# Kernel optimization log

Measured on AMD Instinct MI355X. Metric: run time of the kernel, lower is better.

Reference implementation:

```python
import jax, jax.numpy as jnp
import numpy as np

V, D, F, H, NB, S, B = 16384, 512, 2048, 8, 4, 512, 2
T_STEPS = 3      # config.T: number of PC inference iterations
GAMMA = 0.1      # state-update step size


def _layernorm(x, s, b):
    m = x.mean(-1, keepdims=True)
    v = ((x - m) ** 2).mean(-1, keepdims=True)
    return (x - m) * jax.lax.rsqrt(v + 1e-5) * s + b


def setup_inputs() -> dict:
    key = jax.random.key(0)
    ks = jax.random.split(key, 12)
    r = lambda k, sh: jax.random.normal(k, sh, jnp.float32) * 0.02
    return {
        'word_emb': r(ks[0], (V, D)),
        'pos_emb': r(ks[1], (S, D)),
        'Wq': r(ks[2], (NB, D, D)),
        'Wk': r(ks[3], (NB, D, D)),
        'Wv': r(ks[4], (NB, D, D)),
        'bq': jnp.zeros((NB, D), jnp.float32),
        'bk': jnp.zeros((NB, D), jnp.float32),
        'bv': jnp.zeros((NB, D), jnp.float32),
        'Wo': r(ks[5], (NB, D, D)),
        'bo': jnp.zeros((NB, D), jnp.float32),
        'ln1_s': jnp.ones((NB, D), jnp.float32),
        'ln1_b': jnp.zeros((NB, D), jnp.float32),
        'ln2_s': jnp.ones((NB, D), jnp.float32),
        'ln2_b': jnp.zeros((NB, D), jnp.float32),
        'W1': r(ks[6], (NB, D, F)),
        'b1': jnp.zeros((NB, F), jnp.float32),
        'W2': r(ks[7], (NB, F, D)),
        'b2': jnp.zeros((NB, D), jnp.float32),
        'Wout': r(ks[8], (D, V)),
        'bout': jnp.zeros((V,), jnp.float32),
        'input_ids': jax.random.randint(ks[9], (B, S), 0, V),
        'target_ids': jax.random.randint(ks[10], (B, S), 0, V),
    }


def _forward(word_emb, pos_emb, Wq, Wk, Wv, bq, bk, bv, Wo, bo,
             ln1_s, ln1_b, ln2_s, ln2_b, W1, b1, W2, b2, Wout, bout,
             input_ids, target_ids):
    Bsz, Sl = input_ids.shape
    dh = D // H
    scale = 1.0 / float(np.sqrt(dh))
    ids = jnp.clip(input_ids, 0, V - 1)
    target = jax.nn.one_hot(jnp.clip(target_ids, 0, V - 1), V, dtype=word_emb.dtype)
    # bottom prediction: word + position embeddings
    mu_emb = word_emb[ids] + pos_emb[jnp.arange(Sl)][None]  # (B,S,D)
    causal = jnp.tril(jnp.ones((Sl, Sl), bool))
    neg = jnp.finfo(word_emb.dtype).min

    def attn(x, b):
        h = _layernorm(x, ln1_s[b], ln1_b[b])
        q = (h @ Wq[b] + bq[b]).reshape(Bsz, Sl, H, dh)
        k = (h @ Wk[b] + bk[b]).reshape(Bsz, Sl, H, dh)
        v = (h @ Wv[b] + bv[b]).reshape(Bsz, Sl, H, dh)
        sc = jnp.einsum('bqhd,bkhd->bhqk', q, k) * scale
        sc = jnp.where(causal, sc, neg)
        a = jax.nn.softmax(sc, axis=-1)
        return jnp.einsum('bhqk,bkhd->bqhd', a, v).reshape(Bsz, Sl, D)

    # generative functions g[l]: x_l -> mu_{l+1}; 4 PC layers per block
    # (pc_qkv->attn ctx, pc_output->Wo, pc_layer1->gelu(fc1), pc_layer2->fc2)
    gs = []
    for b in range(NB):
        gs.append(lambda x, b=b: attn(x, b))
        gs.append(lambda x, b=b: x @ Wo[b] + bo[b])
        gs.append(lambda x, b=b: jax.nn.gelu(_layernorm(x, ln2_s[b], ln2_b[b]) @ W1[b] + b1[b]))
        gs.append(lambda x, b=b: x @ W2[b] + b2[b])
    g_top = lambda x: x @ Wout + bout  # output pc layer -> logits mu

    # init_x: forward sweep sets each latent to its prediction
    xs = [mu_emb]
    for g in gs:
        xs.append(g(xs[-1]))
    L = len(gs)

    # T-step iterative PC inference: eps_l = x_l - mu_l, top clamped to target
    # x_l <- x_l + GAMMA * (J_{g_l}(x_l)^T eps_{l+1} - eps_l)
    for _ in range(T_STEPS):
        preds, vjps = [], []
        for l in range(L):
            mu, vj = jax.vjp(gs[l], xs[l])
            preds.append(mu)
            vjps.append(vj)
        logits, vj_top = jax.vjp(g_top, xs[L])
        eps = [xs[0] - mu_emb] + [xs[l + 1] - preds[l] for l in range(L)]
        eps_top = logits - target
        new_xs = []
        for l in range(L + 1):
            td = vjps[l](eps[l + 1])[0] if l < L else vj_top(eps_top)[0]
            new_xs.append(xs[l] + GAMMA * (td - eps[l]))
        xs = new_xs

    return g_top(xs[L])  # get_mu('linear_output')


def reference(word_emb, pos_emb, Wq, Wk, Wv, bq, bk, bv, Wo, bo,
              ln1_s, ln1_b, ln2_s, ln2_b, W1, b1, W2, b2, Wout, bout,
              input_ids, target_ids):
    return _forward(word_emb, pos_emb, Wq, Wk, Wv, bq, bk, bv, Wo, bo,
                    ln1_s, ln1_b, ln2_s, ln2_b, W1, b1, W2, b2, Wout, bout,
                    input_ids, target_ids)
```

## Files before the change

### kernel.cpp

```cpp
#include <hip/hip_runtime.h>
#include <hip/hip_bf16.h>
#include <math.h>

#define D_   512
#define F_   2048
#define V_   16384
#define H_   8
#define DH_  64
#define S_   512
#define B_   2
#define M_   1024
#define MD_  (M_ * D_)
#define MF_  (M_ * F_)
#define GAMMA_ 0.1f

typedef unsigned int u32;
typedef unsigned short u16;
typedef __attribute__((ext_vector_type(4))) float f32x4;
typedef __attribute__((ext_vector_type(8))) short s16x8;
typedef __attribute__((ext_vector_type(4))) u16 u16x4;
typedef __attribute__((ext_vector_type(8))) u16 u16x8;

__device__ __forceinline__ u16 f2b(float f) {
    __hip_bfloat16 h = __float2bfloat16(f);
    return *reinterpret_cast<u16*>(&h);
}
__device__ __forceinline__ float b2f(u16 v) {
    u32 u = ((u32)v) << 16;
    float f; __builtin_memcpy(&f, &u, 4); return f;
}
__device__ __forceinline__ u16x4 pack4(f32x4 v) {
    u16x4 o; o.x = f2b(v[0]); o.y = f2b(v[1]); o.z = f2b(v[2]); o.w = f2b(v[3]);
    return o;
}

__device__ __forceinline__ void gl_lds16(const void* g, void* l) {
    __builtin_amdgcn_global_load_lds((const __attribute__((address_space(1))) u32*)g,
                                     (__attribute__((address_space(3))) u32*)l, 16, 0, 0);
}

__device__ __forceinline__ float gelu_f(float v) {
    float u = 0.7978845608028654f * (v + 0.044715f * v * v * v);
    return 0.5f * v * (1.f + tanhf(u));
}

__device__ __forceinline__ f32x4 xpose4(f32x4 v, int b) {
#pragma unroll
    for (int s = 1; s < 4; s <<= 1) {
        f32x4 nv;
#pragma unroll
        for (int j = 0; j < 4; ++j) {
            float ex = __shfl_xor(v[j ^ s], s, 64);
            nv[j] = ((b ^ j) & s) ? ex : v[j];
        }
        v = nv;
    }
    return v;
}

__device__ __forceinline__ float wave_sum(float v) {
#pragma unroll
    for (int o = 32; o > 0; o >>= 1) v += __shfl_xor(v, o, 64);
    return v;
}

__device__ __forceinline__ void lds_barrier() {
    asm volatile("s_waitcnt lgkmcnt(0)" ::: "memory");
    __builtin_amdgcn_s_barrier();
    __builtin_amdgcn_sched_barrier(0);
}

#define E_F32   0
#define E_GELU  1
#define E_TD    2
#define E_QKV3  3
#define E_OUT   4
#define E_SYM   5

template<int BK>
__device__ __forceinline__ int swz(int c, int row) {
    if constexpr (BK == 32) return c ^ ((row >> 1) & 3);
    else                    return c ^ (row & 7);
}

template<int BM, int BN, int BK, int FM, int FN, int EPI>
__global__ __launch_bounds__(256)
void mfma_gemm(const u16* __restrict__ A, const u16* __restrict__ B,
               float* __restrict__ Cf, u16* __restrict__ Cb,
               u16* __restrict__ Cb2, u16* __restrict__ Cb3,
               const float* __restrict__ bias,
               int K, int lda, int ldb, int ldc,
               long sC, long sKz, float alpha,
               const float* __restrict__ base, const float* __restrict__ subv,
               const float* __restrict__ cvec, const u16* __restrict__ woutTb,
               const int* __restrict__ tcl,
               float* __restrict__ ebF, u16* __restrict__ ebB)
{
    constexpr int WC = BN / (FN * 16);
    static_assert((BM / (FM * 16)) * WC == 4, "4 waves");
    constexpr int LPR = BK / 8;
    constexpr int RPI = 2048 / BK;
    constexpr int NISS = BM / RPI + BN / RPI;
    if constexpr (EPI == E_SYM) {
        if (blockIdx.x > blockIdx.y) return;
    }
    __shared__ __align__(16) u16 Asl[3][BM * BK];
    __shared__ __align__(16) u16 Bsl[3][BN * BK];
    const int t = threadIdx.x, l = t & 63, wid = t >> 6;
    const int m0 = blockIdx.y * BM, n0 = blockIdx.x * BN;
    const long z = blockIdx.z;
    A += z * sKz;
    B += z * sKz;
    if (Cf) Cf += z * sC;

    f32x4 acc[FM][FN] = {};
    const int rm = (wid / WC) * (FM * 16), cn = (wid % WC) * (FN * 16);
    const int lr = l & 15, hi = l >> 4;
    const int srl = t / LPR, sc = t % LPR;

    auto stage = [&](int k0, int pb) {
#pragma unroll
        for (int i = 0; i < BM / RPI; ++i) {
            int row = i * RPI + srl;
            gl_lds16(A + (size_t)(m0 + row) * lda + k0 + swz<BK>(sc, row) * 8,
                     &Asl[pb][i * 2048 + t * 8]);
        }
#pragma unroll
        for (int i = 0; i < BN / RPI; ++i) {
            int row = i * RPI + srl;
            gl_lds16(B + (size_t)(n0 + row) * ldb + k0 + swz<BK>(sc, row) * 8,
                     &Bsl[pb][i * 2048 + t * 8]);
        }
    };
    auto compute = [&](int pb) {
#pragma unroll
        for (int kk = 0; kk < BK / 32; ++kk) {
            s16x8 av[FM], bv[FN];
#pragma unroll
            for (int fm = 0; fm < FM; ++fm)
                av[fm] = *(const s16x8*)&Asl[pb][(rm + fm * 16 + lr) * BK + swz<BK>(kk * 4 + hi, lr) * 8];
#pragma unroll
            for (int fn = 0; fn < FN; ++fn)
                bv[fn] = *(const s16x8*)&Bsl[pb][(cn + fn * 16 + lr) * BK + swz<BK>(kk * 4 + hi, lr) * 8];
#pragma unroll
            for (int fm = 0; fm < FM; ++fm)
#pragma unroll
                for (int fn = 0; fn < FN; ++fn)
                    acc[fm][fn] = __builtin_amdgcn_mfma_f32_16x16x32_bf16(av[fm], bv[fn], acc[fm][fn], 0, 0, 0);
        }
    };

    const int nst = K / BK;
    stage(0, 0);
    if (nst > 1) stage(BK, 1);
    int rd = 0, wr = 2;
    for (int s = 0; s < nst; ++s) {
        if (s < nst - 1)
            asm volatile("s_waitcnt vmcnt(%0)" :: "i"(NISS) : "memory");
        else
            asm volatile("s_waitcnt vmcnt(0)" ::: "memory");
        __builtin_amdgcn_s_barrier();
        __builtin_amdgcn_sched_barrier(0);
        compute(rd);
        if (s + 2 < nst) stage((s + 2) * BK, wr);
        rd = (rd + 1 == 3) ? 0 : rd + 1;
        wr = (wr + 1 == 3) ? 0 : wr + 1;
    }

    const int qb = lr & 3, qi = lr >> 2;
#pragma unroll
    for (int fm = 0; fm < FM; ++fm)
#pragma unroll
        for (int fn = 0; fn < FN; ++fn) {
            const int gm = m0 + rm + fm * 16 + hi * 4 + qb;
            const int gn0 = n0 + cn + fn * 16 + qi * 4;
            const size_t idx0 = (size_t)gm * ldc + gn0;
            if constexpr (EPI == E_QKV3) {
                const int gnf = n0 + cn + fn * 16;
                const int sel = gnf >> 9;
                if (sel < 2) {
                    f32x4 v = xpose4(acc[fm][fn], qb);
                    f32x4 bv4 = *(const f32x4*)&bias[gn0];
#pragma unroll
                    for (int j = 0; j < 4; ++j) v[j] += bv4[j];
                    int b = gm >> 9, s = gm & (S_ - 1);
                    int d9 = gn0 & 511, h = d9 >> 6, d = d9 & 63;
                    u16* dst = (sel == 0) ? Cb : Cb2;
                    *(u16x4*)&dst[(((size_t)(b * H_ + h) * S_ + s) << 6) + d] = pack4(v);
                } else {
                    const int gnl = gnf + lr;
                    const int gm0 = m0 + rm + fm * 16 + hi * 4;
                    int b = gm0 >> 9, s0 = gm0 & (S_ - 1);
                    int d9 = gnl & 511, h = d9 >> 6, d = d9 & 63;
                    float bb = bias[gnl];
                    f32x4 v = acc[fm][fn];
#pragma unroll
                    for (int j = 0; j < 4; ++j) v[j] += bb;
                    *(u16x4*)&Cb3[((((size_t)(b * H_ + h)) << 6) + d) * S_ + s0] = pack4(v);
                }
            } else if constexpr (EPI == E_SYM) {
                const int gnr = n0 + cn + fn * 16 + lr;
                const int mc0 = m0 + rm + fm * 16 + hi * 4;
                *(f32x4*)&Cf[(size_t)gnr * ldc + mc0] = acc[fm][fn];
                f32x4 v = xpose4(acc[fm][fn], qb);
                *(f32x4*)&Cf[idx0] = v;
            } else {
                f32x4 v = xpose4(acc[fm][fn], qb);
                if constexpr (EPI == E_F32) {
#pragma unroll
                    for (int j = 0; j < 4; ++j) v[j] *= alpha;
                    if (bias) {
                        f32x4 bv4 = *(const f32x4*)&bias[gn0];
#pragma unroll
                        for (int j = 0; j < 4; ++j) v[j] += bv4[j];
                    }
                    *(f32x4*)&Cf[idx0] = v;
                    if (Cb) *(u16x4*)&Cb[idx0] = pack4(v);
                } else if constexpr (EPI == E_OUT) {
                    f32x4 bv4 = *(const f32x4*)&bias[gn0];
#pragma unroll
                    for (int j = 0; j < 4; ++j) v[j] += bv4[j];
                    *(f32x4*)&Cf[idx0] = v;
                } else if constexpr (EPI == E_GELU) {
                    f32x4 bv4 = *(const f32x4*)&bias[gn0];
#pragma unroll
                    for (int j = 0; j < 4; ++j) v[j] = gelu_f(v[j] + bv4[j]);
                    *(u16x4*)&Cb[idx0] = pack4(v);
                } else if constexpr (EPI == E_TD) {
                    const int tc = tcl[gm];
                    f32x4 cv4 = *(const f32x4*)&cvec[gn0];
                    f32x4 ba4 = *(const f32x4*)&base[idx0];
                    u16x4 gv = *(const u16x4*)&woutTb[(size_t)tc * D_ + gn0];
                    f32x4 dlt, o2;
#pragma unroll
                    for (int j = 0; j < 4; ++j)
                        dlt[j] = GAMMA_ * (v[j] + cv4[j] - b2f(gv[j]));
                    if (subv) {
                        f32x4 sv4 = *(const f32x4*)&subv[idx0];
#pragma unroll
                        for (int j = 0; j < 4; ++j) dlt[j] -= GAMMA_ * sv4[j];
                    }
#pragma unroll
                    for (int j = 0; j < 4; ++j) o2[j] = ba4[j] + dlt[j];
                    if (Cf) *(f32x4*)&Cf[idx0] = o2;
                    *(u16x4*)&Cb[idx0] = pack4(o2);
                    if (ebF) *(f32x4*)&ebF[idx0] = dlt;
                    if (ebB) *(u16x4*)&ebB[idx0] = pack4(dlt);
                }
            }
        }
}

__global__ __launch_bounds__(256)
void tdec_kernel(const u16* __restrict__ xAb, const u16* __restrict__ Gb,
                 const u16* __restrict__ ebb, const u16* __restrict__ H2b,
                 const float* __restrict__ xAf, const float* __restrict__ ebf,
                 const float* __restrict__ x16f, const float* __restrict__ cvec,
                 const u16* __restrict__ woutTb, const int* __restrict__ tcl,
                 float* __restrict__ xBf, u16* __restrict__ xBb, float* __restrict__ ecf)
{
    constexpr int BM = 32, BN = 64, BK = 64;
    __shared__ __align__(16) u16 Asl[3][BM * BK];
    __shared__ __align__(16) u16 Bsl[3][BN * BK];
    const int t = threadIdx.x, l = t & 63, wid = t >> 6;
    const int m0 = blockIdx.y * BM, n0 = blockIdx.x * BN;
    f32x4 a1[2] = {}, a2[2] = {};
    const int rm = (wid >> 1) * 16, cn = (wid & 1) * 32;
    const int lr = l & 15, hi = l >> 4;
    const int srl = t >> 3, sc = t & 7;

    auto stage = [&](int s, int pb) {
        const u16* A = (s < 8) ? xAb : ebb;
        const u16* B = (s < 8) ? Gb : H2b;
        const int k0 = (s & 7) * BK;
        {
            int row = srl;
            gl_lds16(A + (size_t)(m0 + row) * D_ + k0 + swz<64>(sc, row) * 8,
                     &Asl[pb][t * 8]);
        }
#pragma unroll
        for (int i = 0; i < 2; ++i) {
            int row = i * 32 + srl;
            gl_lds16(B + (size_t)(n0 + row) * D_ + k0 + swz<64>(sc, row) * 8,
                     &Bsl[pb][i * 2048 + t * 8]);
        }
    };
    auto cmp = [&](int pb, f32x4 (&ac)[2]) {
#pragma unroll
        for (int kk = 0; kk < 2; ++kk) {
            s16x8 av = *(const s16x8*)&Asl[pb][(rm + lr) * BK + swz<64>(kk * 4 + hi, lr) * 8];
#pragma unroll
            for (int fn = 0; fn < 2; ++fn) {
                s16x8 bv = *(const s16x8*)&Bsl[pb][(cn + fn * 16 + lr) * BK + swz<64>(kk * 4 + hi, lr) * 8];
                ac[fn] = __builtin_amdgcn_mfma_f32_16x16x32_bf16(av, bv, ac[fn], 0, 0, 0);
            }
        }
    };

    stage(0, 0);
    stage(1, 1);
    int rd = 0, wr = 2;
    for (int s = 0; s < 16; ++s) {
        if (s < 15) asm volatile("s_waitcnt vmcnt(3)" ::: "memory");
        else        asm volatile("s_waitcnt vmcnt(0)" ::: "memory");
        __builtin_amdgcn_s_barrier();
        __builtin_amdgcn_sched_barrier(0);
        if (s < 8) cmp(rd, a1);
        else       cmp(rd, a2);
        if (s + 2 < 16) stage(s + 2, wr);
        rd = (rd + 1 == 3) ? 0 : rd + 1;
        wr = (wr + 1 == 3) ? 0 : wr + 1;
    }

    const int qb = lr & 3, qi = lr >> 2;
#pragma unroll
    for (int fn = 0; fn < 2; ++fn) {
        f32x4 v1 = xpose4(a1[fn], qb);
        f32x4 v2 = xpose4(a2[fn], qb);
        const int gm = m0 + rm + hi * 4 + qb;
        const int gn0 = n0 + cn + fn * 16 + qi * 4;
        const size_t idx0 = (size_t)gm * D_ + gn0;
        const int tc = tcl[gm];
        f32x4 cv4 = *(const f32x4*)&cvec[gn0];
        u16x4 gv = *(const u16x4*)&woutTb[(size_t)tc * D_ + gn0];
        f32x4 xa4 = *(const f32x4*)&xAf[idx0];
        f32x4 eb4 = *(const f32x4*)&ebf[idx0];
        f32x4 x164 = *(const f32x4*)&x16f[idx0];
        f32x4 xb4, ec4;
#pragma unroll
        for (int j = 0; j < 4; ++j) {
            float dlt = GAMMA_ * (v1[j] + cv4[j] - b2f(gv[j]) - eb4[j]);
            xb4[j] = xa4[j] + dlt;
            ec4[j] = xb4[j] - x164[j] - GAMMA_ * v2[j];
        }
        *(f32x4*)&xBf[idx0] = xb4;
        *(u16x4*)&xBb[idx0] = pack4(xb4);
        *(f32x4*)&ecf[idx0] = ec4;
    }
}

__global__ __launch_bounds__(128)
void flash_attn(const u16* __restrict__ q, const u16* __restrict__ k,
                const u16* __restrict__ vT, u16* __restrict__ ctx)
{
    __shared__ __align__(16) u16 Ks[3][64 * 64];
    __shared__ __align__(16) u16 Vs[3][64 * 64];
    __shared__ __align__(16) u16 Ps[2][16 * 64];
    const int t = threadIdx.x, l = t & 63, w = t >> 6;
    const int qt = blockIdx.x, z = blockIdx.y;
    const int bb = z >> 3, hh = z & 7;
    const int lr = l & 15, hi = l >> 4;
    const u16* qp = q + (((size_t)z * S_ + qt * 32 + w * 16) << 6);
    const u16* kp = k + ((size_t)z * S_ << 6);
    const u16* vp = vT + (((size_t)z) << 6) * S_;

    const s16x8 aq0 = *(const s16x8*)&qp[lr * 64 + hi * 8];
    const s16x8 aq1 = *(const s16x8*)&qp[lr * 64 + 32 + hi * 8];

    f32x4 o[4] = {};
    float m[4], ls[4];
#pragma unroll
    for (int r = 0; r < 4; ++r) { m[r] = -3.0e38f; ls[r] = 0.f; }
    const int qrow = qt * 32 + w * 16 + hi * 4;
    const int srow = t >> 3, scl = t & 7;
    const int cg = (scl ^ (srow & 7)) * 8;
    const int sw7 = (lr & 7);
    const int jmax = qt >> 1;

    auto stage = [&](int j, int pb) {
#pragma unroll
        for (int i = 0; i < 4; ++i)
            gl_lds16(kp + ((size_t)(j * 64 + i * 16 + srow) << 6) + cg,
                     &Ks[pb][i * 1024 + t * 8]);
#pragma unroll
        for (int i = 0; i < 4; ++i)
            gl_lds16(vp + (size_t)(i * 16 + srow) * S_ + j * 64 + cg,
                     &Vs[pb][i * 1024 + t * 8]);
    };

    stage(0, 0);
    if (jmax > 0) stage(1, 1);
    int rd = 0, wr = 2;
    for (int j = 0; j <= jmax; ++j) {
        if (j < jmax) asm volatile("s_waitcnt vmcnt(8)" ::: "memory");
        else          asm volatile("s_waitcnt vmcnt(0)" ::: "memory");
        __builtin_amdgcn_s_barrier();
        __builtin_amdgcn_sched_barrier(0);

        float pv[4][4];
        __builtin_amdgcn_s_setprio(1);
#pragma unroll
        for (int fn = 0; fn < 4; ++fn) {
            f32x4 acc = {};
            acc = __builtin_amdgcn_mfma_f32_16x16x32_bf16(aq0,
                    *(const s16x8*)&Ks[rd][((fn * 16 + lr) << 6) + ((hi ^ sw7) * 8)], acc, 0, 0, 0);
            acc = __builtin_amdgcn_mfma_f32_16x16x32_bf16(aq1,
                    *(const s16x8*)&Ks[rd][((fn * 16 + lr) << 6) + (((hi + 4) ^ sw7) * 8)], acc, 0, 0, 0);
#pragma unroll
            for (int r = 0; r < 4; ++r) pv[fn][r] = acc[r] * 0.125f;
        }
        __builtin_amdgcn_s_setprio(0);
        if (j == jmax) {
#pragma unroll
            for (int fn = 0; fn < 4; ++fn) {
                int col = j * 64 + fn * 16 + lr;
#pragma unroll
                for (int r = 0; r < 4; ++r)
                    if (col > qrow + r) pv[fn][r] = -3.0e38f;
            }
        }
        float sc[4], rs[4];
#pragma unroll
        for (int r = 0; r < 4; ++r) {
            float x = fmaxf(fmaxf(pv[0][r], pv[1][r]), fmaxf(pv[2][r], pv[3][r]));
#pragma unroll
            for (int off = 1; off < 16; off <<= 1) x = fmaxf(x, __shfl_xor(x, off, 64));
            float nm = fmaxf(m[r], x);
            sc[r] = expf(m[r] - nm);
            m[r] = nm;
            rs[r] = 0.f;
        }
#pragma unroll
        for (int fn = 0; fn < 4; ++fn)
#pragma unroll
            for (int r = 0; r < 4; ++r) {
                float p = expf(pv[fn][r] - m[r]);
                pv[fn][r] = p;
                rs[r] += p;
            }
#pragma unroll
        for (int r = 0; r < 4; ++r) {
#pragma unroll
            for (int off = 1; off < 16; off <<= 1) rs[r] += __shfl_xor(rs[r], off, 64);
            ls[r] = ls[r] * sc[r] + rs[r];
        }
#pragma unroll
        for (int fn = 0; fn < 4; ++fn)
#pragma unroll
            for (int r = 0; r < 4; ++r) o[fn][r] *= sc[r];
#pragma unroll
        for (int fn = 0; fn < 4; ++fn)
#pragma unroll
            for (int r = 0; r < 4; ++r) {
                int qr = hi * 4 + r;
                int ci = (2 * fn + (lr >> 3)) ^ (qr & 7);
                Ps[w][qr * 64 + ci * 8 + (lr & 7)] = f2b(pv[fn][r]);
            }
        __builtin_amdgcn_s_setprio(1);
#pragma unroll
        for (int ks = 0; ks < 2; ++ks) {
            const s16x8 pa = *(const s16x8*)&Ps[w][lr * 64 + (((4 * ks + hi) ^ sw7) * 8)];
#pragma unroll
            for (int fn = 0; fn < 4; ++fn)
                o[fn] = __builtin_amdgcn_mfma_f32_16x16x32_bf16(pa,
                        *(const s16x8*)&Vs[rd][((fn * 16 + lr) << 6) + (((hi + 4 * ks) ^ sw7) * 8)], o[fn], 0, 0, 0);
        }
        __builtin_amdgcn_s_setprio(0);
        if (j + 2 <= jmax) stage(j + 2, wr);
        rd = (rd + 1 == 3) ? 0 : rd + 1;
        wr = (wr + 1 == 3) ? 0 : wr + 1;
    }
    float inv[4];
#pragma unroll
    for (int r = 0; r < 4; ++r) inv[r] = 1.f / ls[r];
    u16* cp = ctx + ((size_t)(bb * S_ + qt * 32 + w * 16) * D_) + hh * 64;
    const int qb = lr & 3, qi = lr >> 2;
#pragma unroll
    for (int fn = 0; fn < 4; ++fn) {
        f32x4 v = o[fn];
#pragma unroll
        for (int r = 0; r < 4; ++r) v[r] *= inv[r];
        v = xpose4(v, qb);
        *(u16x4*)&cp[(size_t)(hi * 4 + qb) * D_ + fn * 16 + qi * 4] = pack4(v);
    }
}

__global__ __launch_bounds__(256)
void mega_prep(const float* __restrict__ Wq, const float* __restrict__ Wk,
               const float* __restrict__ Wv, const float* __restrict__ Wo,
               const float* __restrict__ W1, const float* __restrict__ W2,
               const float* __restrict__ Wout,
               const float* __restrict__ bq, const float* __restrict__ bk,
               const float* __restrict__ bv, const int* __restrict__ target_ids,
               const float* __restrict__ we, const float* __restrict__ pe,
               const int* __restrict__ input_ids,
               const float* __restrict__ ln1s0, const float* __restrict__ ln1b0,
               u16* __restrict__ wqkvT, u16* __restrict__ woT, u16* __restrict__ w1T,
               u16* __restrict__ w2T, u16* __restrict__ woutT,
               u16* __restrict__ woutD, float* __restrict__ qkvb, int* __restrict__ tcl,
               u16* __restrict__ h_b)
{
    __shared__ float tile[2][64][65];
    __shared__ float sh2[4];
    const int g = blockIdx.x, t = threadIdx.x;

    if (g >= 1281) {
        const int rr = (g - 1281) * 2 + (t >> 7);
        const int lc = t & 127;
        const int ss = rr & (S_ - 1);
        int id = input_ids[rr];
        id = id < 0 ? 0 : (id > V_ - 1 ? V_ - 1 : id);
        const float4 a = ((const float4*)we)[(size_t)id * 128 + lc];
        const float4 b = ((const float4*)pe)[(size_t)ss * 128 + lc];
        float4 x;
        x.x = a.x + b.x; x.y = a.y + b.y; x.z = a.z + b.z; x.w = a.w + b.w;
        const int w = t >> 6, wb = (t >> 7) << 1;
        float s = wave_sum(x.x + x.y + x.z + x.w);
        if ((t & 63) == 0) sh2[w] = s;
        __syncthreads();
        float mu = (sh2[wb] + sh2[wb + 1]) * (1.f / D_);
        float d0 = x.x - mu, d1 = x.y - mu, d2 = x.z - mu, d3 = x.w - mu;
        float qv = wave_sum(d0 * d0 + d1 * d1 + d2 * d2 + d3 * d3);
        __syncthreads();
        if ((t & 63) == 0) sh2[w] = qv;
        __syncthreads();
        float var = (sh2[wb] + sh2[wb + 1]) * (1.f / D_);
        float r = rsqrtf(var + 1e-5f);
        const int c0 = lc * 4;
        float4 scv = *(const float4*)&ln1s0[c0];
        float4 bbv = *(const float4*)&ln1b0[c0];
        f32x4 o;
        o[0] = d0 * r * scv.x + bbv.x; o[1] = d1 * r * scv.y + bbv.y;
        o[2] = d2 * r * scv.z + bbv.z; o[3] = d3 * r * scv.w + bbv.w;
        *(u16x4*)&h_b[(size_t)rr * D_ + c0] = pack4(o);
        return;
    }
    if (g == 1280) {
        for (int i = t; i < M_; i += 256) {
            int v = target_ids[i];
            tcl[i] = v < 0 ? 0 : (v > V_ - 1 ? V_ - 1 : v);
        }
        for (int i = t; i < 4 * 1536; i += 256) {
            int b = i / 1536, j = i - b * 1536;
            qkvb[i] = (j < 512) ? bq[b * 512 + j]
                    : (j < 1024) ? bk[b * 512 + j - 512] : bv[b * 512 + j - 1024];
        }
        return;
    }

    const float* in = nullptr;
    u16 *outT = nullptr, *outC = nullptr;
    int R = 512, C = 512, c0 = 0, rbase = 0;

    if (g < 192) {
        int sel = g / 64, rem = g % 64, zz = rem >> 4, st = (rem >> 1) & 7, hf = rem & 1;
        in = (sel == 0 ? Wq : sel == 1 ? Wk : Wv) + (size_t)zz * 262144;
        outT = wqkvT + (size_t)zz * 786432 + sel * 262144;
        c0 = st * 64; rbase = hf * 256;
    } else if (g < 256) {
        int rem = g - 192, zz = rem >> 4, st = (rem >> 1) & 7, hf = rem & 1;
        in = Wo + (size_t)zz * 262144; outT = woT + (size_t)zz * 262144;
        c0 = st * 64; rbase = hf * 256;
    } else if (g < 512) {
        int rem = g - 256, zz = rem >> 6, sub = rem & 63, st = sub >> 1, hf = sub & 1;
        in = W1 + (size_t)zz * 1048576; outT = w1T + (size_t)zz * 1048576;
        C = 2048; c0 = st * 64; rbase = hf * 256;
    } else if (g < 768) {
        int rem = g - 512, zz = rem >> 6, sub = rem & 63, st = sub & 7, ch = sub >> 3;
        in = W2 + (size_t)zz * 1048576; outT = w2T + (size_t)zz * 1048576;
        R = 2048; c0 = st * 64; rbase = ch * 256;
    } else {
        int rem = g - 768, st = rem >> 1, hf = rem & 1;
        in = Wout; outT = woutT; outC = woutD;
        C = 16384; c0 = st * 64; rbase = hf * 256;
    }

    const int lrow = t >> 4, lcol = (t & 15) * 4;
    float4 va[3][4];
    auto loadit = [&](int it, int slot) {
#pragma unroll
        for (int p = 0; p < 4; ++p)
            va[slot][p] = *(const float4*)&in[(size_t)(rbase + it * 64 + p * 16 + lrow) * C + c0 + lcol];
    };

    loadit(0, 0);
    loadit(1, 1);
#pragma unroll
    for (int it = 0; it < 4; ++it) {
        const int slot = it % 3;
        const int tb = it & 1;
        const int r0 = rbase + it * 64;
#pragma unroll
        for (int p = 0; p < 4; ++p) {
            float4 v = va[slot][p];
            int row = p * 16 + lrow;
            tile[tb][row][lcol] = v.x; tile[tb][row][lcol + 1] = v.y;
            tile[tb][row][lcol + 2] = v.z; tile[tb][row][lcol + 3] = v.w;
            if (outC) {
                f32x4 fv; fv[0] = v.x; fv[1] = v.y; fv[2] = v.z; fv[3] = v.w;
                *(u16x4*)&outC[(size_t)(r0 + row) * C + c0 + lcol] = pack4(fv);
            }
        }
        if (it < 2) loadit(it + 2, (it + 2) % 3);
        lds_barrier();
#pragma unroll
        for (int p = 0; p < 2; ++p) {
            int orow = p * 32 + (t >> 3), oc = (t & 7) * 8;
            u16x8 o;
#pragma unroll
            for (int j = 0; j < 8; ++j) o[j] = f2b(tile[tb][oc + j][orow]);
            *(u16x8*)&outT[(size_t)(c0 + orow) * R + r0 + oc] = o;
        }
    }
}

__global__ __launch_bounds__(256)
void gredcvec(const float* __restrict__ P, u16* __restrict__ G,
              const u16* __restrict__ woutD, const float* __restrict__ bout,
              float* __restrict__ cvec, const u16* __restrict__ w2T3,
              u16* __restrict__ H2)
{
    __shared__ __align__(16) u16 As2[3][32 * 64];
    __shared__ __align__(16) u16 Bs2[3][64 * 64];
    const int blk = blockIdx.x, t = threadIdx.x;
    if (blk < 1024) {
        int i = blk * 256 + t;
        float s = 0.f;
#pragma unroll
        for (int zz = 0; zz < 8; ++zz) s += P[(size_t)zz * D_ * D_ + i];
        G[i] = f2b(s);
    } else if (blk < 1152) {
        const int w = t >> 6, l = t & 63;
        const int d = (blk - 1024) * 4 + w;
        float s = 0.f;
        for (int it = 0; it < 32; ++it) {
            int base = it * 512 + l * 8;
            u16x8 wv = *(const u16x8*)&woutD[(size_t)d * V_ + base];
            float4 b0 = *(const float4*)&bout[base];
            float4 b1 = *(const float4*)&bout[base + 4];
            s += b2f(wv[0]) * b0.x + b2f(wv[1]) * b0.y + b2f(wv[2]) * b0.z + b2f(wv[3]) * b0.w
               + b2f(wv[4]) * b1.x + b2f(wv[5]) * b1.y + b2f(wv[6]) * b1.z + b2f(wv[7]) * b1.w;
        }
        s = wave_sum(s);
        if (l == 0) cvec[d] = s;
    } else {
        const int idx = blk - 1152;
        const int n0 = (idx & 7) * 64, m0 = (idx >> 3) * 32;
        const int l = t & 63, wid = t >> 6;
        const int lr = l & 15, hi = l >> 4;
        const int rm = (wid >> 1) * 16, cn = (wid & 1) * 32;
        const int srl = t >> 3, sc = t & 7;
        f32x4 acc2[2] = {};
        auto stg = [&](int s, int pb) {
            const int k0 = s * 64;
            gl_lds16(w2T3 + (size_t)(m0 + srl) * 2048 + k0 + swz<64>(sc, srl) * 8,
                     &As2[pb][t * 8]);
            gl_lds16(w2T3 + (size_t)(n0 + srl) * 2048 + k0 + swz<64>(sc, srl) * 8,
                     &Bs2[pb][t * 8]);
            gl_lds16(w2T3 + (size_t)(n0 + 32 + srl) * 2048 + k0 + swz<64>(sc, srl) * 8,
                     &Bs2[pb][2048 + t * 8]);
        };
        auto cmp = [&](int pb) {
#pragma unroll
            for (int kk = 0; kk < 2; ++kk) {
                s16x8 av = *(const s16x8*)&As2[pb][(rm + lr) * 64 + swz<64>(kk * 4 + hi, lr) * 8];
#pragma unroll
                for (int fn = 0; fn < 2; ++fn) {
                    s16x8 bv = *(const s16x8*)&Bs2[pb][(cn + fn * 16 + lr) * 64 + swz<64>(kk * 4 + hi, lr) * 8];
                    acc2[fn] = __builtin_amdgcn_mfma_f32_16x16x32_bf16(av, bv, acc2[fn], 0, 0, 0);
                }
            }
        };
        stg(0, 0);
        stg(1, 1);
        int rd = 0, wr = 2;
        for (int s = 0; s < 32; ++s) {
            if (s < 31) asm volatile("s_waitcnt vmcnt(3)" ::: "memory");
            else        asm volatile("s_waitcnt vmcnt(0)" ::: "memory");
            __builtin_amdgcn_s_barrier();
            __builtin_amdgcn_sched_barrier(0);
            cmp(rd);
            if (s + 2 < 32) stg(s + 2, wr);
            rd = (rd + 1 == 3) ? 0 : rd + 1;
            wr = (wr + 1 == 3) ? 0 : wr + 1;
        }
        const int qb = lr & 3, qi = lr >> 2;
#pragma unroll
        for (int fn = 0; fn < 2; ++fn) {
            f32x4 v = xpose4(acc2[fn], qb);
            const int gm = m0 + rm + hi * 4 + qb;
            const int gn0 = n0 + cn + fn * 16 + qi * 4;
            *(u16x4*)&H2[(size_t)gm * D_ + gn0] = pack4(v);
        }
    }
}

__global__ __launch_bounds__(256)
void ln_fwd_kernel(const float* __restrict__ x, const float* __restrict__ s,
                   const float* __restrict__ bb, u16* __restrict__ h)
{
    const int l = threadIdx.x & 63, w = threadIdx.x >> 6;
    const int row = blockIdx.x * 4 + w;
    const float* xr = x + (size_t)row * D_;
    const int c0 = l * 8;
    float4 a = *(const float4*)&xr[c0];
    float4 b = *(const float4*)&xr[c0 + 4];
    float sum = a.x + a.y + a.z + a.w + b.x + b.y + b.z + b.w;
    float mu = wave_sum(sum) * (1.f / D_);
    float d0 = a.x - mu, d1 = a.y - mu, d2 = a.z - mu, d3 = a.w - mu;
    float d4 = b.x - mu, d5 = b.y - mu, d6 = b.z - mu, d7 = b.w - mu;
    float vs = d0*d0 + d1*d1 + d2*d2 + d3*d3 + d4*d4 + d5*d5 + d6*d6 + d7*d7;
    float var = wave_sum(vs) * (1.f / D_);
    float r = rsqrtf(var + 1e-5f);
    float4 s0 = *(const float4*)&s[c0], s1 = *(const float4*)&s[c0 + 4];
    float4 b0 = *(const float4*)&bb[c0], b1 = *(const float4*)&bb[c0 + 4];
    u16* hr = h + (size_t)row * D_;
    f32x4 o0, o1;
    o0[0] = d0 * r * s0.x + b0.x; o0[1] = d1 * r * s0.y + b0.y;
    o0[2] = d2 * r * s0.z + b0.z; o0[3] = d3 * r * s0.w + b0.w;
    o1[0] = d4 * r * s1.x + b1.x; o1[1] = d5 * r * s1.y + b1.y;
    o1[2] = d6 * r * s1.z + b1.z; o1[3] = d7 * r * s1.w + b1.w;
    *(u16x4*)&hr[c0] = pack4(o0);
    *(u16x4*)&hr[c0 + 4] = pack4(o1);
}

extern "C" void kernel_launch(void* const* d_in, const int* in_sizes, int n_in,
                              void* d_out, int out_size, void* d_ws, size_t ws_size,
                              hipStream_t stream)
{
    (void)in_sizes; (void)n_in; (void)out_size;
    const float* Wq  = (const float*)d_in[2];
    const float* Wk  = (const float*)d_in[3];
    const float* Wv  = (const float*)d_in[4];
    const float* bq  = (const float*)d_in[5];
    const float* bk  = (const float*)d_in[6];
    const float* bv  = (const float*)d_in[7];
    const float* Wo  = (const float*)d_in[8];
    const float* bo  = (const float*)d_in[9];
    const float* ln1_s = (const float*)d_in[10];
    const float* ln1_b = (const float*)d_in[11];
    const float* ln2_s = (const float*)d_in[12];
    const float* ln2_b = (const float*)d_in[13];
    const float* W1  = (const float*)d_in[14];
    const float* b1  = (const float*)d_in[15];
    const float* W2  = (const float*)d_in[16];
    const float* b2  = (const float*)d_in[17];
    const float* Wout = (const float*)d_in[18];
    const float* bout = (const float*)d_in[19];
    const int* input_ids  = (const int*)d_in[20];
    const int* target_ids = (const int*)d_in[21];
    float* out = (float*)d_out;

    char* wsb = (char*)d_ws;
    size_t off = 0;
    auto alloc = [&](size_t bytes) -> void* {
        off = (off + 255) & ~(size_t)255;
        void* p = wsb + off; off += bytes; return p;
    };
    u16* wqkvT = (u16*)alloc((size_t)4 * 1536 * D_ * 2);
    u16* woT   = (u16*)alloc((size_t)4 * D_ * D_ * 2);
    u16* w1T   = (u16*)alloc((size_t)4 * D_ * F_ * 2);
    u16* w2T   = (u16*)alloc((size_t)4 * D_ * F_ * 2);
    u16* woutT = (u16*)alloc((size_t)V_ * D_ * 2);
    u16* G_b   = (u16*)alloc((size_t)D_ * D_ * 2);
    u16* H2_b  = (u16*)alloc((size_t)D_ * D_ * 2);
    float* qkvb = (float*)alloc((size_t)4 * 1536 * 4);
    float* bufB = (float*)alloc((size_t)MD_ * 4);
    u16* h_b    = (u16*)alloc((size_t)MD_ * 2);
    u16* gelu_b = (u16*)alloc((size_t)MF_ * 2);
    u16* x16_b  = (u16*)alloc((size_t)MD_ * 2);
    float* cvec = (float*)alloc(D_ * 4);
    int* tcl    = (int*)alloc(M_ * 4);
    size_t uStart = (off + 255) & ~(size_t)255;
    off = uStart;
    u16* woutD   = (u16*)alloc((size_t)V_ * D_ * 2);
    float* Gpart = (float*)alloc((size_t)8 * D_ * D_ * 4);
    size_t endG = off;
    off = uStart;
    u16* q_b   = (u16*)alloc((size_t)MD_ * 2);
    u16* k_b   = (u16*)alloc((size_t)MD_ * 2);
    u16* v_b   = (u16*)alloc((size_t)MD_ * 2);
    u16* ctx_b = (u16*)alloc((size_t)MD_ * 2);
    size_t endA = off;
    off = uStart;
    float* xA  = (float*)alloc((size_t)MD_ * 4);
    float* xB  = (float*)alloc((size_t)MD_ * 4);
    float* eb  = (float*)alloc((size_t)MD_ * 4);
    float* ec  = (float*)alloc((size_t)MD_ * 4);
    u16* xA_b  = (u16*)alloc((size_t)MD_ * 2);
    u16* xB_b  = (u16*)alloc((size_t)MD_ * 2);
    u16* xC_b  = (u16*)alloc((size_t)MD_ * 2);
    u16* eb_b  = (u16*)alloc((size_t)MD_ * 2);
    size_t endT = off;
    size_t need = endG > endA ? endG : endA;
    if (endT > need) need = endT;
    if (need > ws_size) return;

    dim3 blk(256);
    const long NL = 0;
    #define GZ nullptr, nullptr, nullptr, nullptr, nullptr, nullptr, nullptr

    mega_prep<<<dim3(1793), blk, 0, stream>>>(Wq, Wk, Wv, Wo, W1, W2, Wout,
        bq, bk, bv, target_ids, (const float*)d_in[0], (const float*)d_in[1], input_ids,
        ln1_s, ln1_b, wqkvT, woT, w1T, w2T, woutT, woutD, qkvb, tcl, h_b);
    mfma_gemm<128, 128, 64, 4, 4, E_SYM><<<dim3(4, 4, 8), blk, 0, stream>>>(
        woutD, woutD, Gpart, nullptr, nullptr, nullptr, nullptr, 2048, V_, V_, D_,
        (long)D_ * D_, 2048, 1.f, GZ);
    gredcvec<<<dim3(1280), blk, 0, stream>>>(Gpart, G_b, woutD, bout, cvec,
        w2T + (size_t)3 * D_ * F_, H2_b);

    for (int b = 0; b < 4; ++b) {
        const size_t wDD = (size_t)b * D_ * D_, wDF = (size_t)b * D_ * F_;
        if (b)
            ln_fwd_kernel<<<dim3(M_ / 4), blk, 0, stream>>>(bufB, ln1_s + b * D_, ln1_b + b * D_, h_b);
        mfma_gemm<64, 64, 64, 2, 2, E_QKV3><<<dim3(24, 16, 1), blk, 0, stream>>>(
            h_b, wqkvT + (size_t)b * 1536 * 512, nullptr, q_b, k_b, v_b,
            qkvb + b * 1536, D_, D_, D_, 0, NL, NL, 1.f, GZ);
        flash_attn<<<dim3(16, 16), dim3(128), 0, stream>>>(q_b, k_b, v_b, ctx_b);
        mfma_gemm<32, 64, 64, 1, 2, E_F32><<<dim3(8, 32, 1), blk, 0, stream>>>(
            ctx_b, woT + wDD, bufB, nullptr, nullptr, nullptr, bo + b * D_,
            D_, D_, D_, D_, NL, NL, 1.f, GZ);
        ln_fwd_kernel<<<dim3(M_ / 4), blk, 0, stream>>>(bufB, ln2_s + b * D_, ln2_b + b * D_, h_b);
        mfma_gemm<64, 64, 64, 2, 2, E_GELU><<<dim3(32, 16, 1), blk, 0, stream>>>(
            h_b, w1T + wDF, nullptr, gelu_b, nullptr, nullptr, b1 + b * F_,
            D_, D_, D_, F_, NL, NL, 1.f, GZ);
        mfma_gemm<32, 64, 64, 1, 2, E_F32><<<dim3(8, 32, 1), blk, 0, stream>>>(
            gelu_b, w2T + wDF, bufB, (b == 3) ? x16_b : nullptr, nullptr, nullptr, b2 + b * D_,
            F_, F_, F_, D_, NL, NL, 1.f, GZ);
    }

    mfma_gemm<32, 64, 64, 1, 2, E_TD><<<dim3(8, 32, 1), blk, 0, stream>>>(
        x16_b, G_b, xA, xA_b, nullptr, nullptr, nullptr, D_, D_, D_, D_, NL, NL, 1.f,
        bufB, nullptr, cvec, woutT, tcl, eb, eb_b);
    tdec_kernel<<<dim3(8, 32, 1), blk, 0, stream>>>(
        xA_b, G_b, eb_b, H2_b, xA, eb, bufB, cvec, woutT, tcl, xB, xB_b, ec);
    mfma_gemm<32, 64, 64, 1, 2, E_TD><<<dim3(8, 32, 1), blk, 0, stream>>>(
        xB_b, G_b, nullptr, xC_b, nullptr, nullptr, nullptr, D_, D_, D_, D_, NL, NL, 1.f,
        xB, ec, cvec, woutT, tcl, nullptr, nullptr);
    mfma_gemm<128, 128, 32, 4, 4, E_OUT><<<dim3(128, 8, 1), blk, 0, stream>>>(
        xC_b, woutT, out, nullptr, nullptr, nullptr, bout, D_, D_, D_, V_, NL, NL, 1.f, GZ);
    #undef GZ
}
```

Measured before the change: 386.8 us.

## Fuse LayerNorm into QKV and FFN-up GEMMs via an LDS-resident A panel

Adds a new lngemm kernel that loads a 32-row fp32 activation panel, computes LayerNorm statistics in-kernel, and writes the normalized bf16 rows into LDS. It then runs the QKV or W1 GEMM against a triple-buffered B pipeline, with the QKV-split or GELU epilogues moved over from mfma_gemm. This removes the separate ln_fwd_kernel launches and the h_b round trip through global memory; mega_prep now writes raw embeddings to bufB instead of doing LN. The cost is that LN is recomputed by every column block, using smaller 32x64 tiles with twice as many row blocks, and variance is computed one-pass as E[x^2]-mu^2.

```diff
diff --git a/kernel.cpp b/kernel.cpp
--- a/kernel.cpp
+++ b/kernel.cpp
@@ -64,12 +64,6 @@
     return v;
 }
 
-__device__ __forceinline__ void lds_barrier() {
-    asm volatile("s_waitcnt lgkmcnt(0)" ::: "memory");
-    __builtin_amdgcn_s_barrier();
-    __builtin_amdgcn_sched_barrier(0);
-}
-
 #define E_F32   0
 #define E_GELU  1
 #define E_TD    2
@@ -87,7 +81,6 @@
 __global__ __launch_bounds__(256)
 void mfma_gemm(const u16* __restrict__ A, const u16* __restrict__ B,
                float* __restrict__ Cf, u16* __restrict__ Cb,
-               u16* __restrict__ Cb2, u16* __restrict__ Cb3,
                const float* __restrict__ bias,
                int K, int lda, int ldb, int ldc,
                long sC, long sKz, float alpha,
@@ -175,30 +168,7 @@
             const int gm = m0 + rm + fm * 16 + hi * 4 + qb;
             const int gn0 = n0 + cn + fn * 16 + qi * 4;
             const size_t idx0 = (size_t)gm * ldc + gn0;
-            if constexpr (EPI == E_QKV3) {
-                const int gnf = n0 + cn + fn * 16;
-                const int sel = gnf >> 9;
-                if (sel < 2) {
-                    f32x4 v = xpose4(acc[fm][fn], qb);
-                    f32x4 bv4 = *(const f32x4*)&bias[gn0];
-#pragma unroll
-                    for (int j = 0; j < 4; ++j) v[j] += bv4[j];
-                    int b = gm >> 9, s = gm & (S_ - 1);
-                    int d9 = gn0 & 511, h = d9 >> 6, d = d9 & 63;
-                    u16* dst = (sel == 0) ? Cb : Cb2;
-                    *(u16x4*)&dst[(((size_t)(b * H_ + h) * S_ + s) << 6) + d] = pack4(v);
-                } else {
-                    const int gnl = gnf + lr;
-                    const int gm0 = m0 + rm + fm * 16 + hi * 4;
-                    int b = gm0 >> 9, s0 = gm0 & (S_ - 1);
-                    int d9 = gnl & 511, h = d9 >> 6, d = d9 & 63;
-                    float bb = bias[gnl];
-                    f32x4 v = acc[fm][fn];
-#pragma unroll
-                    for (int j = 0; j < 4; ++j) v[j] += bb;
-                    *(u16x4*)&Cb3[((((size_t)(b * H_ + h)) << 6) + d) * S_ + s0] = pack4(v);
-                }
-            } else if constexpr (EPI == E_SYM) {
+            if constexpr (EPI == E_SYM) {
                 const int gnr = n0 + cn + fn * 16 + lr;
                 const int mc0 = m0 + rm + fm * 16 + hi * 4;
                 *(f32x4*)&Cf[(size_t)gnr * ldc + mc0] = acc[fm][fn];
@@ -221,11 +191,6 @@
 #pragma unroll
                     for (int j = 0; j < 4; ++j) v[j] += bv4[j];
                     *(f32x4*)&Cf[idx0] = v;
-                } else if constexpr (EPI == E_GELU) {
-                    f32x4 bv4 = *(const f32x4*)&bias[gn0];
-#pragma unroll
-                    for (int j = 0; j < 4; ++j) v[j] = gelu_f(v[j] + bv4[j]);
-                    *(u16x4*)&Cb[idx0] = pack4(v);
                 } else if constexpr (EPI == E_TD) {
                     const int tc = tcl[gm];
                     f32x4 cv4 = *(const f32x4*)&cvec[gn0];
@@ -249,6 +214,135 @@
                 }
             }
         }
+}
+
+template<int EPI>
+__global__ __launch_bounds__(256)
+void lngemm(const float* __restrict__ X, const u16* __restrict__ B,
+            const float* __restrict__ lns, const float* __restrict__ lnb,
+            const float* __restrict__ bias,
+            u16* __restrict__ Cb, u16* __restrict__ Cb2, u16* __restrict__ Cb3,
+            int ldb_rows , int ldc)
+{
+    __shared__ __align__(16) u16 Apan[32 * 512];
+    __shared__ __align__(16) u16 Bsl[3][64 * 64];
+    const int t = threadIdx.x, l = t & 63, wid = t >> 6;
+    const int m0 = blockIdx.y * 32, n0 = blockIdx.x * 64;
+    const int lr = l & 15, hi = l >> 4;
+    const int rm = (wid >> 1) * 16, cn = (wid & 1) * 32;
+    const int srl = t >> 3, sc = t & 7;
+
+    auto stageB = [&](int s, int pb) {
+#pragma unroll
+        for (int i = 0; i < 2; ++i) {
+            int row = i * 32 + srl;
+            gl_lds16(B + (size_t)(n0 + row) * 512 + s * 64 + swz<64>(sc, row) * 8,
+                     &Bsl[pb][i * 2048 + t * 8]);
+        }
+    };
+    stageB(0, 0);
+    stageB(1, 1);
+
+    {
+        const int row = t >> 3, e8 = t & 7;
+        const float* xr = X + (size_t)(m0 + row) * 512 + e8 * 64;
+        float s1 = 0.f, s2 = 0.f;
+#pragma unroll
+        for (int i = 0; i < 16; ++i) {
+            float4 a = *(const float4*)&xr[i * 4];
+            s1 += a.x + a.y + a.z + a.w;
+            s2 += a.x * a.x + a.y * a.y + a.z * a.z + a.w * a.w;
+        }
+#pragma unroll
+        for (int off = 1; off < 8; off <<= 1) {
+            s1 += __shfl_xor(s1, off, 64);
+            s2 += __shfl_xor(s2, off, 64);
+        }
+        const float mu = s1 * (1.f / 512.f);
+        const float rs = rsqrtf(s2 * (1.f / 512.f) - mu * mu + 1e-5f);
+#pragma unroll
+        for (int i = 0; i < 8; ++i) {
+            float4 a0 = *(const float4*)&xr[i * 8];
+            float4 a1 = *(const float4*)&xr[i * 8 + 4];
+            const int cb = e8 * 64 + i * 8;
+            float4 s0 = *(const float4*)&lns[cb];
+            float4 sB = *(const float4*)&lns[cb + 4];
+            float4 b0 = *(const float4*)&lnb[cb];
+            float4 bB = *(const float4*)&lnb[cb + 4];
+            u16x8 o;
+            o[0] = f2b((a0.x - mu) * rs * s0.x + b0.x);
+            o[1] = f2b((a0.y - mu) * rs * s0.y + b0.y);
+            o[2] = f2b((a0.z - mu) * rs * s0.z + b0.z);
+            o[3] = f2b((a0.w - mu) * rs * s0.w + b0.w);
+            o[4] = f2b((a1.x - mu) * rs * sB.x + bB.x);
+            o[5] = f2b((a1.y - mu) * rs * sB.y + bB.y);
+            o[6] = f2b((a1.z - mu) * rs * sB.z + bB.z);
+            o[7] = f2b((a1.w - mu) * rs * sB.w + bB.w);
+            const int c = e8 * 8 + i;
+            *(u16x8*)&Apan[row * 512 + (c ^ (row & 7)) * 8] = o;
+        }
+    }
+    __syncthreads();
+
+    f32x4 acc[2] = {};
+    int rd = 0, wr = 2;
+    for (int s = 0; s < 8; ++s) {
+        if (s < 7) asm volatile("s_waitcnt vmcnt(2)" ::: "memory");
+        else       asm volatile("s_waitcnt vmcnt(0)" ::: "memory");
+        __builtin_amdgcn_s_barrier();
+        __builtin_amdgcn_sched_barrier(0);
+#pragma unroll
+        for (int kk = 0; kk < 2; ++kk) {
+            const int arow = rm + lr;
+            const int c = s * 8 + kk * 4 + hi;
+            s16x8 av = *(const s16x8*)&Apan[arow * 512 + ((c ^ (arow & 7)) * 8)];
+#pragma unroll
+            for (int fn = 0; fn < 2; ++fn) {
+                s16x8 bv = *(const s16x8*)&Bsl[rd][(cn + fn * 16 + lr) * 64 + swz<64>(kk * 4 + hi, lr) * 8];
+                acc[fn] = __builtin_amdgcn_mfma_f32_16x16x32_bf16(av, bv, acc[fn], 0, 0, 0);
+            }
+        }
+        if (s + 2 < 8) stageB(s + 2, wr);
+        rd = (rd + 1 == 3) ? 0 : rd + 1;
+        wr = (wr + 1 == 3) ? 0 : wr + 1;
+    }
+
+    const int qb = lr & 3, qi = lr >> 2;
+#pragma unroll
+    for (int fn = 0; fn < 2; ++fn) {
+        const int gm = m0 + rm + hi * 4 + qb;
+        const int gn0 = n0 + cn + fn * 16 + qi * 4;
+        if constexpr (EPI == E_QKV3) {
+            const int gnf = n0 + cn + fn * 16;
+            const int sel = gnf >> 9;
+            if (sel < 2) {
+                f32x4 v = xpose4(acc[fn], qb);
+                f32x4 bv4 = *(const f32x4*)&bias[gn0];
+#pragma unroll
+                for (int j = 0; j < 4; ++j) v[j] += bv4[j];
+                int b = gm >> 9, s = gm & (S_ - 1);
+                int d9 = gn0 & 511, h = d9 >> 6, d = d9 & 63;
+                u16* dst = (sel == 0) ? Cb : Cb2;
+                *(u16x4*)&dst[(((size_t)(b * H_ + h) * S_ + s) << 6) + d] = pack4(v);
+            } else {
+                const int gnl = gnf + lr;
+                const int gm0 = m0 + rm + hi * 4;
+                int b = gm0 >> 9, s0 = gm0 & (S_ - 1);
+                int d9 = gnl & 511, h = d9 >> 6, d = d9 & 63;
+                float bb = bias[gnl];
+                f32x4 v = acc[fn];
+#pragma unroll
+                for (int j = 0; j < 4; ++j) v[j] += bb;
+                *(u16x4*)&Cb3[((((size_t)(b * H_ + h)) << 6) + d) * S_ + s0] = pack4(v);
+            }
+        } else {
+            f32x4 v = xpose4(acc[fn], qb);
+            f32x4 bv4 = *(const f32x4*)&bias[gn0];
+#pragma unroll
+            for (int j = 0; j < 4; ++j) v[j] = gelu_f(v[j] + bv4[j]);
+            *(u16x4*)&Cb[(size_t)gm * ldc + gn0] = pack4(v);
+        }
+    }
 }
 
 __global__ __launch_bounds__(256)
@@ -484,14 +578,12 @@
                const float* __restrict__ bv, const int* __restrict__ target_ids,
                const float* __restrict__ we, const float* __restrict__ pe,
                const int* __restrict__ input_ids,
-               const float* __restrict__ ln1s0, const float* __restrict__ ln1b0,
                u16* __restrict__ wqkvT, u16* __restrict__ woT, u16* __restrict__ w1T,
                u16* __restrict__ w2T, u16* __restrict__ woutT,
                u16* __restrict__ woutD, float* __restrict__ qkvb, int* __restrict__ tcl,
-               u16* __restrict__ h_b)
+               float* __restrict__ bufB)
 {
     __shared__ float tile[2][64][65];
-    __shared__ float sh2[4];
     const int g = blockIdx.x, t = threadIdx.x;
 
     if (g >= 1281) {
@@ -504,25 +596,7 @@
         const float4 b = ((const float4*)pe)[(size_t)ss * 128 + lc];
         float4 x;
         x.x = a.x + b.x; x.y = a.y + b.y; x.z = a.z + b.z; x.w = a.w + b.w;
-        const int w = t >> 6, wb = (t >> 7) << 1;
-        float s = wave_sum(x.x + x.y + x.z + x.w);
-        if ((t & 63) == 0) sh2[w] = s;
-        __syncthreads();
-        float mu = (sh2[wb] + sh2[wb + 1]) * (1.f / D_);
-        float d0 = x.x - mu, d1 = x.y - mu, d2 = x.z - mu, d3 = x.w - mu;
-        float qv = wave_sum(d0 * d0 + d1 * d1 + d2 * d2 + d3 * d3);
-        __syncthreads();
-        if ((t & 63) == 0) sh2[w] = qv;
-        __syncthreads();
-        float var = (sh2[wb] + sh2[wb + 1]) * (1.f / D_);
-        float r = rsqrtf(var + 1e-5f);
-        const int c0 = lc * 4;
-        float4 scv = *(const float4*)&ln1s0[c0];
-        float4 bbv = *(const float4*)&ln1b0[c0];
-        f32x4 o;
-        o[0] = d0 * r * scv.x + bbv.x; o[1] = d1 * r * scv.y + bbv.y;
-        o[2] = d2 * r * scv.z + bbv.z; o[3] = d3 * r * scv.w + bbv.w;
-        *(u16x4*)&h_b[(size_t)rr * D_ + c0] = pack4(o);
+        *(float4*)&bufB[(size_t)rr * D_ + lc * 4] = x;
         return;
     }
     if (g == 1280) {
@@ -592,7 +666,9 @@
             }
         }
         if (it < 2) loadit(it + 2, (it + 2) % 3);
-        lds_barrier();
+        asm volatile("s_waitcnt lgkmcnt(0)" ::: "memory");
+        __builtin_amdgcn_s_barrier();
+        __builtin_amdgcn_sched_barrier(0);
 #pragma unroll
         for (int p = 0; p < 2; ++p) {
             int orow = p * 32 + (t >> 3), oc = (t & 7) * 8;
@@ -683,35 +759,6 @@
             *(u16x4*)&H2[(size_t)gm * D_ + gn0] = pack4(v);
         }
     }
-}
-
-__global__ __launch_bounds__(256)
-void ln_fwd_kernel(const float* __restrict__ x, const float* __restrict__ s,
-                   const float* __restrict__ bb, u16* __restrict__ h)
-{
-    const int l = threadIdx.x & 63, w = threadIdx.x >> 6;
-    const int row = blockIdx.x * 4 + w;
-    const float* xr = x + (size_t)row * D_;
-    const int c0 = l * 8;
-    float4 a = *(const float4*)&xr[c0];
-    float4 b = *(const float4*)&xr[c0 + 4];
-    float sum = a.x + a.y + a.z + a.w + b.x + b.y + b.z + b.w;
-    float mu = wave_sum(sum) * (1.f / D_);
-    float d0 = a.x - mu, d1 = a.y - mu, d2 = a.z - mu, d3 = a.w - mu;
-    float d4 = b.x - mu, d5 = b.y - mu, d6 = b.z - mu, d7 = b.w - mu;
-    float vs = d0*d0 + d1*d1 + d2*d2 + d3*d3 + d4*d4 + d5*d5 + d6*d6 + d7*d7;
-    float var = wave_sum(vs) * (1.f / D_);
-    float r = rsqrtf(var + 1e-5f);
-    float4 s0 = *(const float4*)&s[c0], s1 = *(const float4*)&s[c0 + 4];
-    float4 b0 = *(const float4*)&bb[c0], b1 = *(const float4*)&bb[c0 + 4];
-    u16* hr = h + (size_t)row * D_;
-    f32x4 o0, o1;
-    o0[0] = d0 * r * s0.x + b0.x; o0[1] = d1 * r * s0.y + b0.y;
-    o0[2] = d2 * r * s0.z + b0.z; o0[3] = d3 * r * s0.w + b0.w;
-    o1[0] = d4 * r * s1.x + b1.x; o1[1] = d5 * r * s1.y + b1.y;
-    o1[2] = d6 * r * s1.z + b1.z; o1[3] = d7 * r * s1.w + b1.w;
-    *(u16x4*)&hr[c0] = pack4(o0);
-    *(u16x4*)&hr[c0 + 4] = pack4(o1);
 }
 
 extern "C" void kernel_launch(void* const* d_in, const int* in_sizes, int n_in,
@@ -756,7 +803,6 @@
     u16* H2_b  = (u16*)alloc((size_t)D_ * D_ * 2);
     float* qkvb = (float*)alloc((size_t)4 * 1536 * 4);
     float* bufB = (float*)alloc((size_t)MD_ * 4);
-    u16* h_b    = (u16*)alloc((size_t)MD_ * 2);
     u16* gelu_b = (u16*)alloc((size_t)MF_ * 2);
     u16* x16_b  = (u16*)alloc((size_t)MD_ * 2);
     float* cvec = (float*)alloc(D_ * 4);
@@ -792,42 +838,39 @@
 
     mega_prep<<<dim3(1793), blk, 0, stream>>>(Wq, Wk, Wv, Wo, W1, W2, Wout,
         bq, bk, bv, target_ids, (const float*)d_in[0], (const float*)d_in[1], input_ids,
-        ln1_s, ln1_b, wqkvT, woT, w1T, w2T, woutT, woutD, qkvb, tcl, h_b);
+        wqkvT, woT, w1T, w2T, woutT, woutD, qkvb, tcl, bufB);
     mfma_gemm<128, 128, 64, 4, 4, E_SYM><<<dim3(4, 4, 8), blk, 0, stream>>>(
-        woutD, woutD, Gpart, nullptr, nullptr, nullptr, nullptr, 2048, V_, V_, D_,
+        woutD, woutD, Gpart, nullptr, nullptr, 2048, V_, V_, D_,
         (long)D_ * D_, 2048, 1.f, GZ);
     gredcvec<<<dim3(1280), blk, 0, stream>>>(Gpart, G_b, woutD, bout, cvec,
         w2T + (size_t)3 * D_ * F_, H2_b);
 
     for (int b = 0; b < 4; ++b) {
         const size_t wDD = (size_t)b * D_ * D_, wDF = (size_t)b * D_ * F_;
-        if (b)
-            ln_fwd_kernel<<<dim3(M_ / 4), blk, 0, stream>>>(bufB, ln1_s + b * D_, ln1_b + b * D_, h_b);
-        mfma_gemm<64, 64, 64, 2, 2, E_QKV3><<<dim3(24, 16, 1), blk, 0, stream>>>(
-            h_b, wqkvT + (size_t)b * 1536 * 512, nullptr, q_b, k_b, v_b,
-            qkvb + b * 1536, D_, D_, D_, 0, NL, NL, 1.f, GZ);
+        lngemm<E_QKV3><<<dim3(24, 32), blk, 0, stream>>>(
+            bufB, wqkvT + (size_t)b * 1536 * 512, ln1_s + b * D_, ln1_b + b * D_,
+            qkvb + b * 1536, q_b, k_b, v_b, 0, D_);
         flash_attn<<<dim3(16, 16), dim3(128), 0, stream>>>(q_b, k_b, v_b, ctx_b);
         mfma_gemm<32, 64, 64, 1, 2, E_F32><<<dim3(8, 32, 1), blk, 0, stream>>>(
-            ctx_b, woT + wDD, bufB, nullptr, nullptr, nullptr, bo + b * D_,
+            ctx_b, woT + wDD, bufB, nullptr, bo + b * D_,
             D_, D_, D_, D_, NL, NL, 1.f, GZ);
-        ln_fwd_kernel<<<dim3(M_ / 4), blk, 0, stream>>>(bufB, ln2_s + b * D_, ln2_b + b * D_, h_b);
-        mfma_gemm<64, 64, 64, 2, 2, E_GELU><<<dim3(32, 16, 1), blk, 0, stream>>>(
-            h_b, w1T + wDF, nullptr, gelu_b, nullptr, nullptr, b1 + b * F_,
-            D_, D_, D_, F_, NL, NL, 1.f, GZ);
+        lngemm<E_GELU><<<dim3(32, 32), blk, 0, stream>>>(
+            bufB, w1T + wDF, ln2_s + b * D_, ln2_b + b * D_,
+            b1 + b * F_, gelu_b, nullptr, nullptr, 0, F_);
         mfma_gemm<32, 64, 64, 1, 2, E_F32><<<dim3(8, 32, 1), blk, 0, stream>>>(
-            gelu_b, w2T + wDF, bufB, (b == 3) ? x16_b : nullptr, nullptr, nullptr, b2 + b * D_,
+            gelu_b, w2T + wDF, bufB, (b == 3) ? x16_b : nullptr, b2 + b * D_,
             F_, F_, F_, D_, NL, NL, 1.f, GZ);
     }
 
     mfma_gemm<32, 64, 64, 1, 2, E_TD><<<dim3(8, 32, 1), blk, 0, stream>>>(
-        x16_b, G_b, xA, xA_b, nullptr, nullptr, nullptr, D_, D_, D_, D_, NL, NL, 1.f,
+        x16_b, G_b, xA, xA_b, nullptr, D_, D_, D_, D_, NL, NL, 1.f,
         bufB, nullptr, cvec, woutT, tcl, eb, eb_b);
     tdec_kernel<<<dim3(8, 32, 1), blk, 0, stream>>>(
         xA_b, G_b, eb_b, H2_b, xA, eb, bufB, cvec, woutT, tcl, xB, xB_b, ec);
     mfma_gemm<32, 64, 64, 1, 2, E_TD><<<dim3(8, 32, 1), blk, 0, stream>>>(
-        xB_b, G_b, nullptr, xC_b, nullptr, nullptr, nullptr, D_, D_, D_, D_, NL, NL, 1.f,
+        xB_b, G_b, nullptr, xC_b, nullptr, D_, D_, D_, D_, NL, NL, 1.f,
         xB, ec, cvec, woutT, tcl, nullptr, nullptr);
     mfma_gemm<128, 128, 32, 4, 4, E_OUT><<<dim3(128, 8, 1), blk, 0, stream>>>(
-        xC_b, woutT, out, nullptr, nullptr, nullptr, bout, D_, D_, D_, V_, NL, NL, 1.f, GZ);
+        xC_b, woutT, out, nullptr, bout, D_, D_, D_, V_, NL, NL, 1.f, GZ);
     #undef GZ
 }
```

After: 642.7 us. 66.1% more time.
